# Kernel optimization log

Measured on AMD Instinct MI355X. Metric: run time of the kernel, lower is better.

Reference implementation:

```python
import jax, jax.numpy as jnp
import numpy as np
from jax import lax

T = 8192
OBS = 512
HID = 2048
NOBJ = 8


def setup_inputs() -> dict:
    key = jax.random.key(0)
    ks = jax.random.split(key, 9)
    s_in = 1.0 / np.sqrt(OBS)
    s_hid = 1.0 / np.sqrt(HID)
    return {
        "x": jax.random.normal(ks[0], (T, OBS), dtype=jnp.float32),
        "W_in": jax.random.normal(ks[1], (HID, OBS), dtype=jnp.float32) * s_in,
        "W_B": jax.random.normal(ks[2], (HID, OBS), dtype=jnp.float32) * s_in,
        "W_C": jax.random.normal(ks[3], (HID, OBS), dtype=jnp.float32) * s_in,
        "W_delta": jax.random.normal(ks[4], (HID, OBS), dtype=jnp.float32) * s_in,
        "A_log": jax.random.normal(ks[5], (HID,), dtype=jnp.float32),
        "W_out": jax.random.normal(ks[6], (NOBJ, HID), dtype=jnp.float32) * s_hid,
        "b_out": jnp.zeros((NOBJ,), dtype=jnp.float32),
        "W_skip": jax.random.normal(ks[7], (NOBJ, OBS), dtype=jnp.float32) * s_in,
    }


def reference(x, W_in, W_B, W_C, W_delta, A_log, W_out, b_out, W_skip):
    # Input-dependent SSM parameters (4 GEMMs, [T, HID] each)
    x_state = x @ W_in.T
    B = x @ W_B.T
    C = x @ W_C.T
    delta = jax.nn.sigmoid(x @ W_delta.T)
    A = -jnp.exp(A_log)                      # [HID]

    A_bar = jnp.exp(delta * A)               # [T, HID], per-step decay
    Bx = B * x_state                         # [T, HID], per-step input

    def step(h, inp):
        a, bx = inp
        h = a * h + bx
        return h, h

    h0 = jnp.zeros((HID,), dtype=x.dtype)
    _, h_seq = lax.scan(step, h0, (A_bar, Bx))  # [T, HID]

    y = C * h_seq
    out = y @ W_out.T + b_out + x @ W_skip.T    # [T, NOBJ]
    return out
```

## Files before the change

### kernel.cpp

```cpp
#include <hip/hip_runtime.h>
#include <hip/hip_bf16.h>
#include <cstdint>

#define TT   8192
#define KOBS 512
#define HID  2048
#define NOBJ 8
#define NCH  64
#define CT   128

typedef unsigned short u16;
typedef uint32_t u32;
typedef short bf16x8 __attribute__((ext_vector_type(8)));
typedef float f32x4  __attribute__((ext_vector_type(4)));
typedef unsigned short u16x4 __attribute__((ext_vector_type(4)));
typedef unsigned short u16x8 __attribute__((ext_vector_type(8)));

static __device__ __forceinline__ float bf2f(u16 u) {
    union { uint32_t i; float f; } v;
    v.i = ((uint32_t)u) << 16;
    return v.f;
}
static __device__ __forceinline__ u16 f2bf(float f) {
    union { float f; uint32_t i; } v;
    v.f = f;
    uint32_t lsb = (v.i >> 16) & 1u;
    uint32_t r = v.i + 0x7fffu + lsb;
    return (u16)(r >> 16);
}

static __device__ __forceinline__ void async_ld16(const u16* g, u16* l) {
    __builtin_amdgcn_global_load_lds(
        (const __attribute__((address_space(1))) uint32_t*)g,
        (__attribute__((address_space(3))) uint32_t*)l,
        16, 0, 0);
}

__launch_bounds__(256)
__global__ void prep_all(const float* __restrict__ x,
                         const float* __restrict__ Win,
                         const float* __restrict__ WB,
                         const float* __restrict__ WC,
                         const float* __restrict__ Wd,
                         const float* __restrict__ A_log,
                         const float* __restrict__ b_out,
                         const float* __restrict__ W_skip,
                         float* __restrict__ out,
                         u16* __restrict__ x_bf,
                         u16* __restrict__ W_bf,
                         float* __restrict__ A_e)
{
    if (blockIdx.x < 512) {
        const int wave = threadIdx.x >> 6;
        const int lane = threadIdx.x & 63;
        const int t0 = (blockIdx.x * 4 + wave) * 4;

        float acc[4][NOBJ];
#pragma unroll
        for (int tt = 0; tt < 4; tt++)
#pragma unroll
            for (int o = 0; o < NOBJ; o++) acc[tt][o] = 0.f;

#pragma unroll
        for (int i = 0; i < 2; i++) {
            const int kv = (i * 64 + lane) * 4;
            float4 w[NOBJ];
#pragma unroll
            for (int o = 0; o < NOBJ; o++)
                w[o] = *(const float4*)(W_skip + (size_t)o * KOBS + kv);
#pragma unroll
            for (int tt = 0; tt < 4; tt++) {
                const size_t off = (size_t)(t0 + tt) * KOBS + kv;
                float4 xv = *(const float4*)(x + off);
                u16x4 xb = { f2bf(xv.x), f2bf(xv.y), f2bf(xv.z), f2bf(xv.w) };
                *(u16x4*)&x_bf[off] = xb;
#pragma unroll
                for (int o = 0; o < NOBJ; o++)
                    acc[tt][o] += xv.x * w[o].x + xv.y * w[o].y +
                                  xv.z * w[o].z + xv.w * w[o].w;
            }
        }
#pragma unroll
        for (int s = 32; s > 0; s >>= 1)
#pragma unroll
            for (int tt = 0; tt < 4; tt++)
#pragma unroll
                for (int o = 0; o < NOBJ; o++)
                    acc[tt][o] += __shfl_xor(acc[tt][o], s, 64);
        if (lane == 0) {
#pragma unroll
            for (int tt = 0; tt < 4; tt++)
#pragma unroll
                for (int o = 0; o < NOBJ; o++)
                    out[(size_t)(t0 + tt) * NOBJ + o] = acc[tt][o] + b_out[o];
        }
    } else {
        const int tid0 = (blockIdx.x - 512) * 256 + threadIdx.x;
#pragma unroll
        for (int q = 0; q < 2; q++) {
            const int i = tid0 + q * 262144;
            int n  = i >> 6;
            int k8 = (i & 63) * 8;
            int h  = n >> 2;
            int w  = n & 3;
            const float* src = (w == 0) ? Win : (w == 1) ? WB
                             : (w == 2) ? WC  : Wd;
            const float4* s4 = (const float4*)(src + (size_t)h * KOBS + k8);
            float4 a = s4[0], b = s4[1];
            u16x4 o1 = { f2bf(a.x), f2bf(a.y), f2bf(a.z), f2bf(a.w) };
            u16x4 o2 = { f2bf(b.x), f2bf(b.y), f2bf(b.z), f2bf(b.w) };
            *(u16x4*)&W_bf[(size_t)i * 8]     = o1;
            *(u16x4*)&W_bf[(size_t)i * 8 + 4] = o2;
        }
        if (tid0 < HID)
            A_e[tid0] = -__expf(A_log[tid0]) * 1.44269504f;
    }
}

__launch_bounds__(256, 6)
__global__ void gemm_fused(const u16* __restrict__ x_bf,
                           const u16* __restrict__ W_bf,
                           const float* __restrict__ A_e,
                           const float* __restrict__ W_out,
                           u16* __restrict__ YC,
                           u16* __restrict__ Ptl16,
                           float* __restrict__ P,
                           float* __restrict__ S)
{
    __shared__ __align__(16) u16 smem[3 * 128 * 40];
    __shared__ float Ps[256], Ss[256];
    u16* a_s = smem;
    u16* b_s = smem + 4096;

    const int tid  = threadIdx.x;
    const int bm   = blockIdx.x & 63;
    const int bn   = blockIdx.x >> 6;
    const int m0t  = bm * 128;
    const int n0   = bn * 128;
    const int lane = tid & 63;
    const int wave = tid >> 6;
    const int wn   = (wave & 1) * 64;
    const int wt   = (wave >> 1) * 64;
    const int fr   = lane & 15;
    const int fq   = lane >> 4;

    f32x4 acc[4][4];
#pragma unroll
    for (int i = 0; i < 4; i++)
#pragma unroll
        for (int j = 0; j < 4; j++) {
            f32x4 z = {0.f, 0.f, 0.f, 0.f};
            acc[i][j] = z;
        }

    const int srow = tid >> 2;
    const int scg  = (tid & 3) ^ ((srow >> 1) & 3);
    const u16* gA0 = x_bf + (size_t)(m0t + srow) * KOBS + scg * 8;
    const u16* gA1 = gA0 + (size_t)64 * KOBS;
    const u16* gB0 = W_bf + (size_t)(n0 + srow) * KOBS + scg * 8;
    const u16* gB1 = gB0 + (size_t)64 * KOBS;
    u16* lA0 = &a_s[tid * 8];
    u16* lA1 = &a_s[2048 + tid * 8];
    u16* lB0 = &b_s[tid * 8];
    u16* lB1 = &b_s[2048 + tid * 8];

    const int pcg = fq ^ ((fr >> 1) & 3);

    for (int kb = 0; kb < KOBS; kb += 32) {
        async_ld16(gA0 + kb, lA0);
        async_ld16(gA1 + kb, lA1);
        async_ld16(gB0 + kb, lB0);
        async_ld16(gB1 + kb, lB1);
        __syncthreads();

        bf16x8 af[4], bfx[4];
#pragma unroll
        for (int i = 0; i < 4; i++)
            af[i] = *(const bf16x8*)&b_s[(wn + i * 16 + fr) * 32 + pcg * 8];
#pragma unroll
        for (int j = 0; j < 4; j++)
            bfx[j] = *(const bf16x8*)&a_s[(wt + j * 16 + fr) * 32 + pcg * 8];

#pragma unroll
        for (int i = 0; i < 4; i++)
#pragma unroll
            for (int j = 0; j < 4; j++)
                acc[i][j] = __builtin_amdgcn_mfma_f32_16x16x32_bf16(
                    af[i], bfx[j], acc[i][j], 0, 0, 0);
        __syncthreads();
    }

    const int hq = wn >> 2;
#pragma unroll
    for (int i = 0; i < 4; i++) {
        const int hl = hq + i * 4 + fq;
        const float ae = A_e[bn * 32 + hl];
#pragma unroll
        for (int j = 0; j < 4; j++) {
            const int tl = wt + j * 16 + fr;
            f32x4 v = acc[i][j];
            float sig = 1.0f / (1.0f + __expf(-v[3]));
            smem[(0 * 128 + tl) * 40 + hl] = f2bf(v[0] * v[1]);
            smem[(1 * 128 + tl) * 40 + hl] = f2bf(v[2]);
            smem[(2 * 128 + tl) * 40 + hl] = f2bf(sig * ae);
        }
    }
    __syncthreads();

    {
        const int hi  = tid & 31;
        const int seg = tid >> 5;
        float p = 1.f, s = 0.f;
        const int tbase = seg * 16;
#pragma unroll
        for (int t = 0; t < 16; t++) {
            const int row = tbase + t;
            float a  = exp2f(bf2f(smem[(2 * 128 + row) * 40 + hi]));
            float bx = bf2f(smem[(0 * 128 + row) * 40 + hi]);
            s = fmaf(a, s, bx);
            p *= a;
            smem[(0 * 128 + row) * 40 + hi] = f2bf(s);
            smem[(2 * 128 + row) * 40 + hi] = f2bf(p);
        }
        Ps[seg * 32 + hi] = p;
        Ss[seg * 32 + hi] = s;
    }
    __syncthreads();

    if (tid < 32) {
        float rr = 1.f, sr = 0.f;
#pragma unroll
        for (int sg = 0; sg < 8; sg++) {
            float ps = Ps[sg * 32 + tid], ss = Ss[sg * 32 + tid];
            Ps[sg * 32 + tid] = rr;
            Ss[sg * 32 + tid] = sr;
            sr = fmaf(ps, sr, ss);
            rr *= ps;
        }
        P[(size_t)bm * HID + bn * 32 + tid] = rr;
        S[(size_t)bm * HID + bn * 32 + tid] = sr;
    }
    __syncthreads();

#pragma unroll
    for (int it = 0; it < 2; it++) {
        const int idx = it * 256 + tid;
        const int t   = idx >> 2;
        const int cg  = idx & 3;
        const int sg  = t >> 4;
        u16x8 s8  = *(const u16x8*)&smem[(0 * 128 + t) * 40 + cg * 8];
        u16x8 r8  = *(const u16x8*)&smem[(2 * 128 + t) * 40 + cg * 8];
        u16x8 cc8 = *(const u16x8*)&smem[(1 * 128 + t) * 40 + cg * 8];
        u16x8 yb8, yc8;
#pragma unroll
        for (int e = 0; e < 8; e++) {
            float Sp = Ss[sg * 32 + cg * 8 + e];
            float Rp = Ps[sg * 32 + cg * 8 + e];
            float sv = bf2f(s8[e]);
            float rv = bf2f(r8[e]);
            float cc = bf2f(cc8[e]);
            yb8[e] = f2bf(cc * fmaf(rv, Sp, sv));
            yc8[e] = f2bf(cc * rv * Rp);
        }
        *(u16x8*)(YC + (size_t)(m0t + t) * HID + bn * 32 + cg * 8) = yc8;
        *(u16x8*)&smem[(0 * 128 + t) * 40 + cg * 8] = yb8;
    }
    __syncthreads();

    bf16x8 wfrag = {0, 0, 0, 0, 0, 0, 0, 0};
    if (fr < 8) {
        const float* wp = W_out + (size_t)fr * HID + bn * 32 + fq * 8;
        float4 wa = *(const float4*)wp;
        float4 wb = *(const float4*)(wp + 4);
        wfrag[0] = (short)f2bf(wa.x); wfrag[1] = (short)f2bf(wa.y);
        wfrag[2] = (short)f2bf(wa.z); wfrag[3] = (short)f2bf(wa.w);
        wfrag[4] = (short)f2bf(wb.x); wfrag[5] = (short)f2bf(wb.y);
        wfrag[6] = (short)f2bf(wb.z); wfrag[7] = (short)f2bf(wb.w);
    }
#pragma unroll
    for (int mt = 0; mt < 2; mt++) {
        const int tb = wave * 32 + mt * 16;
        bf16x8 yfrag = *(const bf16x8*)&smem[(0 * 128 + tb + fr) * 40 + fq * 8];
        f32x4 pacc = {0.f, 0.f, 0.f, 0.f};
        pacc = __builtin_amdgcn_mfma_f32_16x16x32_bf16(wfrag, yfrag, pacc,
                                                       0, 0, 0);
        if (fq < 2) {
            u16x4 pv = { f2bf(pacc[0]), f2bf(pacc[1]),
                         f2bf(pacc[2]), f2bf(pacc[3]) };
            *(u16x4*)&Ptl16[((size_t)bn * TT + m0t + tb + fr) * NOBJ + 4 * fq]
                = pv;
        }
    }
}

__launch_bounds__(256)
__global__ void combine_reduce(const float* __restrict__ P,
                               const float* __restrict__ S,
                               float* __restrict__ H0,
                               const u16* __restrict__ Ptl16,
                               float* __restrict__ out)
{
    if (blockIdx.x < 8) {
        const int h = blockIdx.x * 256 + threadIdx.x;
        float hrun = 0.f;
#pragma unroll 8
        for (int c = 0; c < NCH; c++) {
            H0[c * HID + h] = hrun;
            hrun = fmaf(P[c * HID + h], hrun, S[c * HID + h]);
        }
    } else {
        const int rb = blockIdx.x - 8;
        const int t  = rb * 128 + (threadIdx.x >> 1);
        const int q  = threadIdx.x & 1;
        float sum0 = 0.f, sum1 = 0.f, sum2 = 0.f, sum3 = 0.f;
#pragma unroll 8
        for (int bn = 0; bn < 64; bn++) {
            u16x4 v = *(const u16x4*)
                &Ptl16[((size_t)bn * TT + t) * NOBJ + q * 4];
            sum0 += bf2f(v[0]); sum1 += bf2f(v[1]);
            sum2 += bf2f(v[2]); sum3 += bf2f(v[3]);
        }
        float4* op = (float4*)&out[(size_t)t * NOBJ + q * 4];
        float4 cur = *op;
        cur.x += sum0; cur.y += sum1; cur.z += sum2; cur.w += sum3;
        *op = cur;
    }
}

__launch_bounds__(256)
__global__ void final_out(const u16* __restrict__ YC,
                          const float* __restrict__ H0,
                          const float* __restrict__ W_out,
                          float* __restrict__ out)
{
    __shared__ __align__(16) u16 ybuf[64 * 256];
    __shared__ __align__(16) u16 wst[8 * 264];
    __shared__ float h0s[256];
    const int tid  = threadIdx.x;
    const int tc   = blockIdx.x >> 3;
    const int hg   = blockIdx.x & 7;
    const int lane = tid & 63;
    const int wave = tid >> 6;
    const int fr   = lane & 15;
    const int fq   = lane >> 4;
    const int t0   = tc * 64;

#pragma unroll
    for (int o = 0; o < 8; o++)
        wst[o * 264 + tid] = f2bf(W_out[(size_t)o * HID + hg * 256 + tid]);
    h0s[tid] = H0[(size_t)(tc >> 1) * HID + hg * 256 + tid];
    __syncthreads();

    const int g   = tid & 31;
    const int tb0 = tid >> 5;
    float4 h0a = *(const float4*)&h0s[g * 8];
    float4 h0b = *(const float4*)&h0s[g * 8 + 4];
    const float h0r[8] = { h0a.x, h0a.y, h0a.z, h0a.w,
                           h0b.x, h0b.y, h0b.z, h0b.w };
#pragma unroll
    for (int k = 0; k < 8; k++) {
        const int t = tb0 + k * 8;
        const size_t off = (size_t)(t0 + t) * HID + hg * 256 + g * 8;
        bf16x8 yc = *(const bf16x8*)(YC + off);
        bf16x8 yv;
#pragma unroll
        for (int e = 0; e < 8; e++)
            yv[e] = (short)f2bf(bf2f((u16)yc[e]) * h0r[e]);
        *(bf16x8*)&ybuf[t * 256 + ((g ^ (t & 7)) << 3)] = yv;
    }
    __syncthreads();

    bf16x8 bw[8];
#pragma unroll
    for (int ks = 0; ks < 8; ks++) {
        bf16x8 w = {0, 0, 0, 0, 0, 0, 0, 0};
        if (fr < 8)
            w = *(const bf16x8*)&wst[fr * 264 + ks * 32 + fq * 8];
        bw[ks] = w;
    }

    {
        const int t = wave * 16 + fr;
        f32x4 acc2 = {0.f, 0.f, 0.f, 0.f};
#pragma unroll
        for (int ks = 0; ks < 8; ks++) {
            const int gg = ks * 4 + fq;
            bf16x8 yv = *(const bf16x8*)
                &ybuf[t * 256 + ((gg ^ (fr & 7)) << 3)];
            acc2 = __builtin_amdgcn_mfma_f32_16x16x32_bf16(bw[ks], yv, acc2,
                                                           0, 0, 0);
        }
        if (fq < 2) {
            const int tg = t0 + t;
#pragma unroll
            for (int reg = 0; reg < 4; reg++)
                atomicAdd(&out[(size_t)tg * NOBJ + 4 * fq + reg], acc2[reg]);
        }
    }
}

extern "C" void kernel_launch(void* const* d_in, const int* in_sizes, int n_in,
                              void* d_out, int out_size, void* d_ws, size_t ws_size,
                              hipStream_t stream)
{
    const float* x      = (const float*)d_in[0];
    const float* Win    = (const float*)d_in[1];
    const float* WB     = (const float*)d_in[2];
    const float* WC     = (const float*)d_in[3];
    const float* Wd     = (const float*)d_in[4];
    const float* A_log  = (const float*)d_in[5];
    const float* W_out  = (const float*)d_in[6];
    const float* b_out  = (const float*)d_in[7];
    const float* W_skip = (const float*)d_in[8];
    float* out = (float*)d_out;

    char* ws = (char*)d_ws;
    size_t off = 0;
    auto alloc = [&](size_t bytes) -> void* {
        void* p = (void*)(ws + off);
        off += (bytes + 255) & ~(size_t)255;
        return p;
    };

    u16*   x_bf  = (u16*)  alloc((size_t)TT * KOBS * 2);
    u16*   W_bf  = (u16*)  alloc((size_t)4 * HID * KOBS * 2);
    float* A_e   = (float*)alloc((size_t)HID * 4);
    u16*   YC    = (u16*)  alloc((size_t)TT * HID * 2);
    u16*   Ptl16 = (u16*)  alloc((size_t)64 * TT * NOBJ * 2);
    float* P     = (float*)alloc((size_t)NCH * HID * 4);
    float* S     = (float*)alloc((size_t)NCH * HID * 4);
    float* H0    = (float*)alloc((size_t)NCH * HID * 4);
    (void)ws_size; (void)in_sizes; (void)n_in; (void)out_size;

    prep_all<<<1536, 256, 0, stream>>>(x, Win, WB, WC, Wd, A_log,
                                       b_out, W_skip, out, x_bf, W_bf, A_e);
    gemm_fused<<<4096, 256, 0, stream>>>(x_bf, W_bf, A_e, W_out,
                                         YC, Ptl16, P, S);
    combine_reduce<<<72, 256, 0, stream>>>(P, S, H0, Ptl16, out);
    final_out<<<1024, 256, 0, stream>>>(YC, H0, W_out, out);
}
```

Measured before the change: 207.0 us.

## Double GEMM K-step to 64 and swizzle block order for L2 locality

The fused GEMM main loop now loads 64-wide K slices per iteration (two MFMA sub-steps), with an 8-way XOR swizzle in LDS. This halves the number of barrier pairs and loop iterations. Block indices are also remapped into 8x8 super-tiles so that concurrently running blocks share x and W rows in L2. The LDS buffer grows to 32 KB, which may reduce how many blocks fit per CU.

```diff
diff --git a/kernel.cpp b/kernel.cpp
--- a/kernel.cpp
+++ b/kernel.cpp
@@ -127,14 +127,16 @@
                            float* __restrict__ P,
                            float* __restrict__ S)
 {
-    __shared__ __align__(16) u16 smem[3 * 128 * 40];
+    __shared__ __align__(16) u16 smem[16384];
     __shared__ float Ps[256], Ss[256];
     u16* a_s = smem;
-    u16* b_s = smem + 4096;
+    u16* b_s = smem + 8192;
 
     const int tid  = threadIdx.x;
-    const int bm   = blockIdx.x & 63;
-    const int bn   = blockIdx.x >> 6;
+    const int sg   = blockIdx.x >> 6;
+    const int wi   = blockIdx.x & 63;
+    const int bm   = (sg & 7) * 8 + (wi & 7);
+    const int bn   = (sg >> 3) * 8 + (wi >> 3);
     const int m0t  = bm * 128;
     const int n0   = bn * 128;
     const int lane = tid & 63;
@@ -153,40 +155,39 @@
             acc[i][j] = z;
         }
 
-    const int srow = tid >> 2;
-    const int scg  = (tid & 3) ^ ((srow >> 1) & 3);
-    const u16* gA0 = x_bf + (size_t)(m0t + srow) * KOBS + scg * 8;
-    const u16* gA1 = gA0 + (size_t)64 * KOBS;
-    const u16* gB0 = W_bf + (size_t)(n0 + srow) * KOBS + scg * 8;
-    const u16* gB1 = gB0 + (size_t)64 * KOBS;
-    u16* lA0 = &a_s[tid * 8];
-    u16* lA1 = &a_s[2048 + tid * 8];
-    u16* lB0 = &b_s[tid * 8];
-    u16* lB1 = &b_s[2048 + tid * 8];
-
-    const int pcg = fq ^ ((fr >> 1) & 3);
-
-    for (int kb = 0; kb < KOBS; kb += 32) {
-        async_ld16(gA0 + kb, lA0);
-        async_ld16(gA1 + kb, lA1);
-        async_ld16(gB0 + kb, lB0);
-        async_ld16(gB1 + kb, lB1);
+    const int srow8 = tid >> 3;
+    const int scg   = (tid & 7) ^ (srow8 & 7);
+    const u16* gA = x_bf + (size_t)(m0t + srow8) * KOBS + scg * 8;
+    const u16* gB = W_bf + (size_t)(n0 + srow8) * KOBS + scg * 8;
+    u16* lA = &a_s[tid * 8];
+    u16* lB = &b_s[tid * 8];
+
+    for (int kb = 0; kb < KOBS; kb += 64) {
+#pragma unroll
+        for (int p = 0; p < 4; p++) {
+            async_ld16(gA + (size_t)p * 32 * KOBS + kb, lA + p * 2048);
+            async_ld16(gB + (size_t)p * 32 * KOBS + kb, lB + p * 2048);
+        }
         __syncthreads();
 
-        bf16x8 af[4], bfx[4];
-#pragma unroll
-        for (int i = 0; i < 4; i++)
-            af[i] = *(const bf16x8*)&b_s[(wn + i * 16 + fr) * 32 + pcg * 8];
-#pragma unroll
-        for (int j = 0; j < 4; j++)
-            bfx[j] = *(const bf16x8*)&a_s[(wt + j * 16 + fr) * 32 + pcg * 8];
-
-#pragma unroll
-        for (int i = 0; i < 4; i++)
+#pragma unroll
+        for (int ks = 0; ks < 2; ks++) {
+            const int pcg = (ks * 4 + fq) ^ (fr & 7);
+            bf16x8 af[4], bfx[4];
+#pragma unroll
+            for (int i = 0; i < 4; i++)
+                af[i] = *(const bf16x8*)&b_s[(wn + i * 16 + fr) * 64 + pcg * 8];
 #pragma unroll
             for (int j = 0; j < 4; j++)
-                acc[i][j] = __builtin_amdgcn_mfma_f32_16x16x32_bf16(
-                    af[i], bfx[j], acc[i][j], 0, 0, 0);
+                bfx[j] = *(const bf16x8*)&a_s[(wt + j * 16 + fr) * 64 + pcg * 8];
+
+#pragma unroll
+            for (int i = 0; i < 4; i++)
+#pragma unroll
+                for (int j = 0; j < 4; j++)
+                    acc[i][j] = __builtin_amdgcn_mfma_f32_16x16x32_bf16(
+                        af[i], bfx[j], acc[i][j], 0, 0, 0);
+        }
         __syncthreads();
     }
 
@@ -230,10 +231,10 @@
     if (tid < 32) {
         float rr = 1.f, sr = 0.f;
 #pragma unroll
-        for (int sg = 0; sg < 8; sg++) {
-            float ps = Ps[sg * 32 + tid], ss = Ss[sg * 32 + tid];
-            Ps[sg * 32 + tid] = rr;
-            Ss[sg * 32 + tid] = sr;
+        for (int sgg = 0; sgg < 8; sgg++) {
+            float ps = Ps[sgg * 32 + tid], ss = Ss[sgg * 32 + tid];
+            Ps[sgg * 32 + tid] = rr;
+            Ss[sgg * 32 + tid] = sr;
             sr = fmaf(ps, sr, ss);
             rr *= ps;
         }
@@ -247,15 +248,15 @@
         const int idx = it * 256 + tid;
         const int t   = idx >> 2;
         const int cg  = idx & 3;
-        const int sg  = t >> 4;
+        const int sgg = t >> 4;
         u16x8 s8  = *(const u16x8*)&smem[(0 * 128 + t) * 40 + cg * 8];
         u16x8 r8  = *(const u16x8*)&smem[(2 * 128 + t) * 40 + cg * 8];
         u16x8 cc8 = *(const u16x8*)&smem[(1 * 128 + t) * 40 + cg * 8];
         u16x8 yb8, yc8;
 #pragma unroll
         for (int e = 0; e < 8; e++) {
-            float Sp = Ss[sg * 32 + cg * 8 + e];
-            float Rp = Ps[sg * 32 + cg * 8 + e];
+            float Sp = Ss[sgg * 32 + cg * 8 + e];
+            float Rp = Ps[sgg * 32 + cg * 8 + e];
             float sv = bf2f(s8[e]);
             float rv = bf2f(r8[e]);
             float cc = bf2f(cc8[e]);
```

Result: faster. 193.2 us (-6.7%).
